# Optimization experiments

Measured on AMD Instinct MI355X. Metric: run time of the kernel, lower is better.

## Reference

```python
import jax, jax.numpy as jnp
import numpy as np

# NSAFlowLayer config (from init_kwargs)
W_ORTHO = 0.5      # w: blend weight of soft-polar retraction
MAX_ITER = 50      # max_iter (run fixed-length under jit; tol check omitted)
LR = 0.1           # 'default' initial learning rate for the fidelity gradient step
NS_ITERS = 8       # Newton-Schulz iterations for the (k,k) inverse matrix sqrt
EPS = 1e-8

B, P, K = 32, 16384, 64


def _invsqrt_ns(M):
    """Differentiable inverse sqrt of SPD (k,k) matrix via coupled Newton-Schulz."""
    k = M.shape[0]
    I = jnp.eye(k, dtype=M.dtype)
    nrm = jnp.trace(M) + EPS
    Y = M / nrm
    Z = I
    for _ in range(NS_ITERS):  # small fixed loop over k x k mats
        T = 0.5 * (3.0 * I - Z @ Y)
        Y = Y @ T
        Z = T @ Z
    return Z / jnp.sqrt(nrm)  # approx M^{-1/2}


def _nsa_flow_single(x0):
    """One independent NSA flow: gradient step on 0.5||Y-X0||^2, soft-polar
    retraction toward the Stiefel manifold, nonnegativity projection."""
    def step(Y, _):
        G = Y - x0                      # fidelity gradient (p,k)
        Y = Y - LR * G                  # gradient step
        S = _invsqrt_ns(Y.T @ Y)        # (k,k) inverse sqrt of Gram matrix
        Y = (1.0 - W_ORTHO) * Y + W_ORTHO * (Y @ S)  # soft polar retraction
        Y = jnp.maximum(Y, 0.0)         # nonneg projection
        return Y, None
    Yf, _ = jax.lax.scan(step, x0, None, length=MAX_ITER)  # Y0 = X0
    return Yf


def setup_inputs() -> dict:
    key = jax.random.key(0)
    X0 = jax.random.uniform(key, (B, P, K), dtype=jnp.float32)
    return {"X0": X0}


def reference(X0) -> jnp.ndarray:
    return jax.vmap(_nsa_flow_single)(X0)  # (B, p, k)
```

## Files before the change

### kernel.cpp

```cpp
#include <hip/hip_runtime.h>


#define BATCH 32
#define NP    16384
#define NK    64
#define NITER 50
#define NSIT  8
#define EPSC  1e-8f

#define BPB   16
#define RPB   (NP / BPB)
#define CH    64
#define NCH   (RPB / CH)
#define NBLK  (BATCH * BPB)
#define NT    256

#define FMA16(D, A0, A1, A2, A3, BV) do {                                  \
  D[0][0] = fmaf(A0, BV.x, D[0][0]); D[0][1] = fmaf(A0, BV.y, D[0][1]);    \
  D[0][2] = fmaf(A0, BV.z, D[0][2]); D[0][3] = fmaf(A0, BV.w, D[0][3]);    \
  D[1][0] = fmaf(A1, BV.x, D[1][0]); D[1][1] = fmaf(A1, BV.y, D[1][1]);    \
  D[1][2] = fmaf(A1, BV.z, D[1][2]); D[1][3] = fmaf(A1, BV.w, D[1][3]);    \
  D[2][0] = fmaf(A2, BV.x, D[2][0]); D[2][1] = fmaf(A2, BV.y, D[2][1]);    \
  D[2][2] = fmaf(A2, BV.z, D[2][2]); D[2][3] = fmaf(A2, BV.w, D[2][3]);    \
  D[3][0] = fmaf(A3, BV.x, D[3][0]); D[3][1] = fmaf(A3, BV.y, D[3][1]);    \
  D[3][2] = fmaf(A3, BV.z, D[3][2]); D[3][3] = fmaf(A3, BV.w, D[3][3]);    \
} while (0)

__device__ __forceinline__ void gram_acc(const float (*sZ)[NK], int i0, int j0,
                                         float (&acc)[4][4]) {
#pragma unroll 4
  for (int r = 0; r < CH; ++r) {
    float4 zi = *(const float4*)&sZ[r][i0];
    float4 zj = *(const float4*)&sZ[r][j0];
    FMA16(acc, zi.x, zi.y, zi.z, zi.w, zj);
  }
}

__global__ __launch_bounds__(NT, 2) void k_init(const float* __restrict__ X0,
                                                float* __restrict__ Y,
                                                float* __restrict__ partials) {
  __shared__ float sZ[CH][NK];
  const int tid = threadIdx.x, blk = blockIdx.x;
  const int b = blk >> 4, rb = blk & 15;
  const size_t base = ((size_t)b * NP + (size_t)rb * RPB) * NK;
  const float* __restrict__ x0 = X0 + base;
  float* __restrict__ y = Y + base;
  const int it = tid >> 4, jt = tid & 15;
  const int i0 = it * 4, j0 = jt * 4;
  float acc[4][4] = {{0.f}};

  for (int ch = 0; ch < NCH; ++ch) {
    const float* xo = x0 + ch * CH * NK;
    float* yo = y + ch * CH * NK;
#pragma unroll
    for (int q = 0; q < 4; ++q) {
      int fi = (q * NT + tid) * 4;
      float4 xv = *(const float4*)(xo + fi);
      *(float4*)(yo + fi) = xv;
      int r = fi >> 6, c = fi & 63;
      *(float4*)&sZ[r][c] = xv;
    }
    __syncthreads();
    gram_acc(sZ, i0, j0, acc);
    __syncthreads();
  }
  float* p = partials + (size_t)blk * NK * NK;
#pragma unroll
  for (int a = 0; a < 4; ++a)
    *(float4*)(p + (i0 + a) * NK + j0) =
        make_float4(acc[a][0], acc[a][1], acc[a][2], acc[a][3]);
}

__global__ void k_ns(const float* __restrict__ partials, float* __restrict__ S) {
  __shared__ float sA[NK][68];
  __shared__ float sB[NK][68];
  __shared__ float sT[NK][68];
  __shared__ float sRed[16];

  const int tid = threadIdx.x, b = blockIdx.x;
  const int it = tid >> 4, jt = tid & 15;
  const int i0 = it * 4, j0 = jt * 4;

  float m[4][4] = {{0.f}};
  const float* pb = partials + (size_t)b * BPB * NK * NK;
#pragma unroll
  for (int p = 0; p < BPB; ++p) {
    const float* pp = pb + p * NK * NK;
#pragma unroll
    for (int a = 0; a < 4; ++a) {
      float4 v = *(const float4*)(pp + (i0 + a) * NK + j0);
      m[a][0] += v.x; m[a][1] += v.y; m[a][2] += v.z; m[a][3] += v.w;
    }
  }
  if (it == jt) sRed[it] = m[0][0] + m[1][1] + m[2][2] + m[3][3];
  __syncthreads();
  float nrm = EPSC;
#pragma unroll
  for (int i = 0; i < 16; ++i) nrm += sRed[i];
  const float inv = 1.0f / nrm;

#pragma unroll
  for (int a = 0; a < 4; ++a)
#pragma unroll
    for (int c = 0; c < 4; ++c) {
      sA[i0 + a][j0 + c] = m[a][c] * inv;
      sB[i0 + a][j0 + c] = (i0 + a) == (j0 + c) ? 1.0f : 0.0f;
    }
  __syncthreads();

  for (int ns = 0; ns < NSIT; ++ns) {
    float d[4][4] = {{0.f}};
#pragma unroll 4
    for (int k = 0; k < NK; ++k) {
      float b0 = sB[i0 + 0][k], b1 = sB[i0 + 1][k];
      float b2 = sB[i0 + 2][k], b3 = sB[i0 + 3][k];
      float4 av = *(const float4*)&sA[k][j0];
      FMA16(d, b0, b1, b2, b3, av);
    }
#pragma unroll
    for (int a = 0; a < 4; ++a)
#pragma unroll
      for (int c = 0; c < 4; ++c)
        sT[i0 + a][j0 + c] =
            (((i0 + a) == (j0 + c)) ? 1.5f : 0.0f) - 0.5f * d[a][c];
    __syncthreads();

    float r1[4][4] = {{0.f}}, r2[4][4] = {{0.f}};
#pragma unroll 4
    for (int k = 0; k < NK; ++k) {
      float y0 = sA[i0 + 0][k], y1 = sA[i0 + 1][k];
      float y2 = sA[i0 + 2][k], y3 = sA[i0 + 3][k];
      float4 tv = *(const float4*)&sT[k][j0];
      FMA16(r1, y0, y1, y2, y3, tv);
      float t0 = sT[i0 + 0][k], t1 = sT[i0 + 1][k];
      float t2 = sT[i0 + 2][k], t3 = sT[i0 + 3][k];
      float4 zv = *(const float4*)&sB[k][j0];
      FMA16(r2, t0, t1, t2, t3, zv);
    }
    __syncthreads();
#pragma unroll
    for (int a = 0; a < 4; ++a)
#pragma unroll
      for (int c = 0; c < 4; ++c) {
        sA[i0 + a][j0 + c] = r1[a][c];
        sB[i0 + a][j0 + c] = r2[a][c];
      }
    __syncthreads();
  }

  const float sc = 1.0f / sqrtf(nrm);
  float* Sb = S + (size_t)b * NK * NK;
#pragma unroll
  for (int a = 0; a < 4; ++a) {
    float4 v = make_float4(sB[i0 + a][j0 + 0] * sc, sB[i0 + a][j0 + 1] * sc,
                           sB[i0 + a][j0 + 2] * sc, sB[i0 + a][j0 + 3] * sc);
    *(float4*)(Sb + (i0 + a) * NK + j0) = v;
  }
}

__global__ __launch_bounds__(NT, 2) void k_fused(const float* __restrict__ X0,
                                                 float* __restrict__ Y,
                                                 const float* __restrict__ S,
                                                 float* __restrict__ partials,
                                                 int last) {
  __shared__ float sS[NK][NK];
  __shared__ float sYp[CH][NK + 1];
  __shared__ float sZ[CH][NK];

  const int tid = threadIdx.x, blk = blockIdx.x;
  const int b = blk >> 4, rb = blk & 15;
  const size_t base = ((size_t)b * NP + (size_t)rb * RPB) * NK;
  const float* __restrict__ x0 = X0 + base;
  float* __restrict__ y = Y + base;

  {
    const float4* Sb = (const float4*)(S + (size_t)b * NK * NK);
    float4* d = (float4*)sS;
    for (int i = tid; i < NK * NK / 4; i += NT) d[i] = Sb[i];
  }

  const int it = tid >> 4, jt = tid & 15;
  const int i0 = it * 4, j0 = jt * 4;
  float acc[4][4] = {{0.f}};
  __syncthreads();

  for (int ch = 0; ch < NCH; ++ch) {
    const float* xo = x0 + ch * CH * NK;
    float* yo = y + ch * CH * NK;

#pragma unroll
    for (int q = 0; q < 4; ++q) {
      int fi = (q * NT + tid) * 4;
      int r = fi >> 6, c = fi & 63;
      float4 yv = *(const float4*)(yo + fi);
      float4 xv = *(const float4*)(xo + fi);
      sYp[r][c + 0] = fmaf(0.9f, yv.x, 0.1f * xv.x);
      sYp[r][c + 1] = fmaf(0.9f, yv.y, 0.1f * xv.y);
      sYp[r][c + 2] = fmaf(0.9f, yv.z, 0.1f * xv.z);
      sYp[r][c + 3] = fmaf(0.9f, yv.w, 0.1f * xv.w);
    }
    __syncthreads();

    float dot[4][4] = {{0.f}};
#pragma unroll 4
    for (int k = 0; k < NK; ++k) {
      float a0 = sYp[i0 + 0][k], a1 = sYp[i0 + 1][k];
      float a2 = sYp[i0 + 2][k], a3 = sYp[i0 + 3][k];
      float4 bv = *(const float4*)&sS[k][j0];
      FMA16(dot, a0, a1, a2, a3, bv);
    }

#pragma unroll
    for (int a = 0; a < 4; ++a) {
      int r = i0 + a;
      float4 yn;
      yn.x = fmaxf(fmaf(0.5f, sYp[r][j0 + 0], 0.5f * dot[a][0]), 0.f);
      yn.y = fmaxf(fmaf(0.5f, sYp[r][j0 + 1], 0.5f * dot[a][1]), 0.f);
      yn.z = fmaxf(fmaf(0.5f, sYp[r][j0 + 2], 0.5f * dot[a][2]), 0.f);
      yn.w = fmaxf(fmaf(0.5f, sYp[r][j0 + 3], 0.5f * dot[a][3]), 0.f);
      *(float4*)(yo + r * NK + j0) = yn;
      if (!last) {
        float4 xv = *(const float4*)(xo + r * NK + j0);
        float4 z;
        z.x = fmaf(0.9f, yn.x, 0.1f * xv.x);
        z.y = fmaf(0.9f, yn.y, 0.1f * xv.y);
        z.z = fmaf(0.9f, yn.z, 0.1f * xv.z);
        z.w = fmaf(0.9f, yn.w, 0.1f * xv.w);
        *(float4*)&sZ[r][j0] = z;
      }
    }
    __syncthreads();
    if (!last) gram_acc(sZ, i0, j0, acc);
    __syncthreads();
  }

  if (!last) {
    float* p = partials + (size_t)blk * NK * NK;
#pragma unroll
    for (int a = 0; a < 4; ++a)
      *(float4*)(p + (i0 + a) * NK + j0) =
          make_float4(acc[a][0], acc[a][1], acc[a][2], acc[a][3]);
  }
}

extern "C" void kernel_launch(void* const* d_in, const int* in_sizes, int n_in,
                              void* d_out, int out_size, void* d_ws,
                              size_t ws_size, hipStream_t stream) {
  (void)in_sizes; (void)n_in; (void)out_size; (void)ws_size;
  const float* X0 = (const float*)d_in[0];
  float* Y = (float*)d_out;
  float* partials = (float*)d_ws;
  float* S = partials + (size_t)NBLK * NK * NK;

  k_init<<<NBLK, NT, 0, stream>>>(X0, Y, partials);
  for (int t = 0; t < NITER; ++t) {
    k_ns<<<BATCH, NT, 0, stream>>>(partials, S);
    k_fused<<<NBLK, NT, 0, stream>>>(X0, Y, S, partials, t == NITER - 1 ? 1 : 0);
  }
}
```

Before: 10.58 ms.

## Double row-blocks per batch, widen NS kernel, reuse LDS buffer, peel first NS step

When the workspace is large enough, each batch's P rows are split across 32 blocks instead of 16, doubling the grid so more CUs stay busy. LDS use in the fused kernel drops by reusing the sYp buffer for the Gram input, and occupancy bounds rise to 4 blocks per CU. The Newton-Schulz kernel now runs 512 threads with 2x4 tiles, reduces the trace with a wave shuffle, and peels the first iteration since Z starts as the identity. In exchange there are twice as many partial Gram matrices to sum, plus an extra barrier per chunk, and the fast path depends on the workspace size.

```diff
diff --git a/kernel.cpp b/kernel.cpp
--- a/kernel.cpp
+++ b/kernel.cpp
@@ -7,13 +7,10 @@
 #define NITER 50
 #define NSIT  8
 #define EPSC  1e-8f
-
-#define BPB   16
-#define RPB   (NP / BPB)
 #define CH    64
-#define NCH   (RPB / CH)
-#define NBLK  (BATCH * BPB)
 #define NT    256
+#define NTNS  512
+#define SP    68
 
 #define FMA16(D, A0, A1, A2, A3, BV) do {                                  \
   D[0][0] = fmaf(A0, BV.x, D[0][0]); D[0][1] = fmaf(A0, BV.y, D[0][1]);    \
@@ -26,7 +23,14 @@
   D[3][2] = fmaf(A3, BV.z, D[3][2]); D[3][3] = fmaf(A3, BV.w, D[3][3]);    \
 } while (0)
 
-__device__ __forceinline__ void gram_acc(const float (*sZ)[NK], int i0, int j0,
+#define FMA8(D, A0, A1, BV) do {                                           \
+  D[0][0] = fmaf(A0, BV.x, D[0][0]); D[0][1] = fmaf(A0, BV.y, D[0][1]);    \
+  D[0][2] = fmaf(A0, BV.z, D[0][2]); D[0][3] = fmaf(A0, BV.w, D[0][3]);    \
+  D[1][0] = fmaf(A1, BV.x, D[1][0]); D[1][1] = fmaf(A1, BV.y, D[1][1]);    \
+  D[1][2] = fmaf(A1, BV.z, D[1][2]); D[1][3] = fmaf(A1, BV.w, D[1][3]);    \
+} while (0)
+
+__device__ __forceinline__ void gram_acc(const float (*sZ)[SP], int i0, int j0,
                                          float (&acc)[4][4]) {
 #pragma unroll 4
   for (int r = 0; r < CH; ++r) {
@@ -36,20 +40,23 @@
   }
 }
 
-__global__ __launch_bounds__(NT, 2) void k_init(const float* __restrict__ X0,
+__global__ __launch_bounds__(NT, 4) void k_init(const float* __restrict__ X0,
                                                 float* __restrict__ Y,
-                                                float* __restrict__ partials) {
-  __shared__ float sZ[CH][NK];
+                                                float* __restrict__ partials,
+                                                int shift) {
+  __shared__ float sZ[CH][SP];
   const int tid = threadIdx.x, blk = blockIdx.x;
-  const int b = blk >> 4, rb = blk & 15;
-  const size_t base = ((size_t)b * NP + (size_t)rb * RPB) * NK;
+  const int bpb = 1 << shift;
+  const int b = blk >> shift, rb = blk & (bpb - 1);
+  const int rpb = NP >> shift, nch = rpb / CH;
+  const size_t base = ((size_t)b * NP + (size_t)rb * rpb) * NK;
   const float* __restrict__ x0 = X0 + base;
   float* __restrict__ y = Y + base;
   const int it = tid >> 4, jt = tid & 15;
   const int i0 = it * 4, j0 = jt * 4;
   float acc[4][4] = {{0.f}};
 
-  for (int ch = 0; ch < NCH; ++ch) {
+  for (int ch = 0; ch < nch; ++ch) {
     const float* xo = x0 + ch * CH * NK;
     float* yo = y + ch * CH * NK;
 #pragma unroll
@@ -71,36 +78,46 @@
         make_float4(acc[a][0], acc[a][1], acc[a][2], acc[a][3]);
 }
 
-__global__ void k_ns(const float* __restrict__ partials, float* __restrict__ S) {
-  __shared__ float sA[NK][68];
-  __shared__ float sB[NK][68];
-  __shared__ float sT[NK][68];
-  __shared__ float sRed[16];
+__global__ __launch_bounds__(NTNS, 2) void k_ns(const float* __restrict__ partials,
+                                                float* __restrict__ S,
+                                                int npart) {
+  __shared__ float sA[NK][SP];
+  __shared__ float sB[NK][SP];
+  __shared__ float sT[NK][SP];
+  __shared__ float sRed[8];
 
   const int tid = threadIdx.x, b = blockIdx.x;
   const int it = tid >> 4, jt = tid & 15;
-  const int i0 = it * 4, j0 = jt * 4;
-
-  float m[4][4] = {{0.f}};
-  const float* pb = partials + (size_t)b * BPB * NK * NK;
-#pragma unroll
-  for (int p = 0; p < BPB; ++p) {
+  const int i0 = it * 2, j0 = jt * 4;
+
+  float m[2][4] = {{0.f}};
+  const float* pb = partials + (size_t)b * npart * NK * NK;
+#pragma unroll 4
+  for (int p = 0; p < npart; ++p) {
     const float* pp = pb + p * NK * NK;
 #pragma unroll
-    for (int a = 0; a < 4; ++a) {
+    for (int a = 0; a < 2; ++a) {
       float4 v = *(const float4*)(pp + (i0 + a) * NK + j0);
       m[a][0] += v.x; m[a][1] += v.y; m[a][2] += v.z; m[a][3] += v.w;
     }
   }
-  if (it == jt) sRed[it] = m[0][0] + m[1][1] + m[2][2] + m[3][3];
+  float local = 0.f;
+#pragma unroll
+  for (int a = 0; a < 2; ++a)
+#pragma unroll
+    for (int c = 0; c < 4; ++c)
+      if ((i0 + a) == (j0 + c)) local += m[a][c];
+#pragma unroll
+  for (int off = 32; off; off >>= 1) local += __shfl_down(local, off);
+  if ((tid & 63) == 0) sRed[tid >> 6] = local;
   __syncthreads();
   float nrm = EPSC;
 #pragma unroll
-  for (int i = 0; i < 16; ++i) nrm += sRed[i];
+  for (int w = 0; w < 8; ++w) nrm += sRed[w];
   const float inv = 1.0f / nrm;
 
 #pragma unroll
-  for (int a = 0; a < 4; ++a)
+  for (int a = 0; a < 2; ++a)
 #pragma unroll
     for (int c = 0; c < 4; ++c) {
       sA[i0 + a][j0 + c] = m[a][c] * inv;
@@ -108,38 +125,61 @@
     }
   __syncthreads();
 
-  for (int ns = 0; ns < NSIT; ++ns) {
-    float d[4][4] = {{0.f}};
+  {
+#pragma unroll
+    for (int a = 0; a < 2; ++a)
+#pragma unroll
+      for (int c = 0; c < 4; ++c)
+        sT[i0 + a][j0 + c] =
+            (((i0 + a) == (j0 + c)) ? 1.5f : 0.0f) - 0.5f * sA[i0 + a][j0 + c];
+    __syncthreads();
+    float r1[2][4] = {{0.f}};
+#pragma unroll 4
+    for (int k = 0; k < NK; ++k) {
+      float y0 = sA[i0 + 0][k], y1 = sA[i0 + 1][k];
+      float4 tv = *(const float4*)&sT[k][j0];
+      FMA8(r1, y0, y1, tv);
+    }
+    __syncthreads();
+#pragma unroll
+    for (int a = 0; a < 2; ++a)
+#pragma unroll
+      for (int c = 0; c < 4; ++c) {
+        sA[i0 + a][j0 + c] = r1[a][c];
+        sB[i0 + a][j0 + c] = sT[i0 + a][j0 + c];
+      }
+    __syncthreads();
+  }
+
+  for (int ns = 1; ns < NSIT; ++ns) {
+    float d[2][4] = {{0.f}};
 #pragma unroll 4
     for (int k = 0; k < NK; ++k) {
       float b0 = sB[i0 + 0][k], b1 = sB[i0 + 1][k];
-      float b2 = sB[i0 + 2][k], b3 = sB[i0 + 3][k];
       float4 av = *(const float4*)&sA[k][j0];
-      FMA16(d, b0, b1, b2, b3, av);
-    }
-#pragma unroll
-    for (int a = 0; a < 4; ++a)
+      FMA8(d, b0, b1, av);
+    }
+#pragma unroll
+    for (int a = 0; a < 2; ++a)
 #pragma unroll
       for (int c = 0; c < 4; ++c)
         sT[i0 + a][j0 + c] =
             (((i0 + a) == (j0 + c)) ? 1.5f : 0.0f) - 0.5f * d[a][c];
     __syncthreads();
 
-    float r1[4][4] = {{0.f}}, r2[4][4] = {{0.f}};
+    float r1[2][4] = {{0.f}}, r2[2][4] = {{0.f}};
 #pragma unroll 4
     for (int k = 0; k < NK; ++k) {
       float y0 = sA[i0 + 0][k], y1 = sA[i0 + 1][k];
-      float y2 = sA[i0 + 2][k], y3 = sA[i0 + 3][k];
       float4 tv = *(const float4*)&sT[k][j0];
-      FMA16(r1, y0, y1, y2, y3, tv);
+      FMA8(r1, y0, y1, tv);
       float t0 = sT[i0 + 0][k], t1 = sT[i0 + 1][k];
-      float t2 = sT[i0 + 2][k], t3 = sT[i0 + 3][k];
       float4 zv = *(const float4*)&sB[k][j0];
-      FMA16(r2, t0, t1, t2, t3, zv);
-    }
-    __syncthreads();
-#pragma unroll
-    for (int a = 0; a < 4; ++a)
+      FMA8(r2, t0, t1, zv);
+    }
+    __syncthreads();
+#pragma unroll
+    for (int a = 0; a < 2; ++a)
 #pragma unroll
       for (int c = 0; c < 4; ++c) {
         sA[i0 + a][j0 + c] = r1[a][c];
@@ -151,25 +191,26 @@
   const float sc = 1.0f / sqrtf(nrm);
   float* Sb = S + (size_t)b * NK * NK;
 #pragma unroll
-  for (int a = 0; a < 4; ++a) {
+  for (int a = 0; a < 2; ++a) {
     float4 v = make_float4(sB[i0 + a][j0 + 0] * sc, sB[i0 + a][j0 + 1] * sc,
                            sB[i0 + a][j0 + 2] * sc, sB[i0 + a][j0 + 3] * sc);
     *(float4*)(Sb + (i0 + a) * NK + j0) = v;
   }
 }
 
-__global__ __launch_bounds__(NT, 2) void k_fused(const float* __restrict__ X0,
+__global__ __launch_bounds__(NT, 4) void k_fused(const float* __restrict__ X0,
                                                  float* __restrict__ Y,
                                                  const float* __restrict__ S,
                                                  float* __restrict__ partials,
-                                                 int last) {
+                                                 int last, int shift) {
   __shared__ float sS[NK][NK];
-  __shared__ float sYp[CH][NK + 1];
-  __shared__ float sZ[CH][NK];
+  __shared__ float sYp[CH][SP];
 
   const int tid = threadIdx.x, blk = blockIdx.x;
-  const int b = blk >> 4, rb = blk & 15;
-  const size_t base = ((size_t)b * NP + (size_t)rb * RPB) * NK;
+  const int bpb = 1 << shift;
+  const int b = blk >> shift, rb = blk & (bpb - 1);
+  const int rpb = NP >> shift, nch = rpb / CH;
+  const size_t base = ((size_t)b * NP + (size_t)rb * rpb) * NK;
   const float* __restrict__ x0 = X0 + base;
   float* __restrict__ y = Y + base;
 
@@ -184,7 +225,7 @@
   float acc[4][4] = {{0.f}};
   __syncthreads();
 
-  for (int ch = 0; ch < NCH; ++ch) {
+  for (int ch = 0; ch < nch; ++ch) {
     const float* xo = x0 + ch * CH * NK;
     float* yo = y + ch * CH * NK;
 
@@ -194,10 +235,12 @@
       int r = fi >> 6, c = fi & 63;
       float4 yv = *(const float4*)(yo + fi);
       float4 xv = *(const float4*)(xo + fi);
-      sYp[r][c + 0] = fmaf(0.9f, yv.x, 0.1f * xv.x);
-      sYp[r][c + 1] = fmaf(0.9f, yv.y, 0.1f * xv.y);
-      sYp[r][c + 2] = fmaf(0.9f, yv.z, 0.1f * xv.z);
-      sYp[r][c + 3] = fmaf(0.9f, yv.w, 0.1f * xv.w);
+      float4 yp;
+      yp.x = fmaf(0.9f, yv.x, 0.1f * xv.x);
+      yp.y = fmaf(0.9f, yv.y, 0.1f * xv.y);
+      yp.z = fmaf(0.9f, yv.z, 0.1f * xv.z);
+      yp.w = fmaf(0.9f, yv.w, 0.1f * xv.w);
+      *(float4*)&sYp[r][c] = yp;
     }
     __syncthreads();
 
@@ -209,15 +252,17 @@
       float4 bv = *(const float4*)&sS[k][j0];
       FMA16(dot, a0, a1, a2, a3, bv);
     }
+    __syncthreads();
 
 #pragma unroll
     for (int a = 0; a < 4; ++a) {
       int r = i0 + a;
+      float4 ypv = *(const float4*)&sYp[r][j0];
       float4 yn;
-      yn.x = fmaxf(fmaf(0.5f, sYp[r][j0 + 0], 0.5f * dot[a][0]), 0.f);
-      yn.y = fmaxf(fmaf(0.5f, sYp[r][j0 + 1], 0.5f * dot[a][1]), 0.f);
-      yn.z = fmaxf(fmaf(0.5f, sYp[r][j0 + 2], 0.5f * dot[a][2]), 0.f);
-      yn.w = fmaxf(fmaf(0.5f, sYp[r][j0 + 3], 0.5f * dot[a][3]), 0.f);
+      yn.x = fmaxf(fmaf(0.5f, ypv.x, 0.5f * dot[a][0]), 0.f);
+      yn.y = fmaxf(fmaf(0.5f, ypv.y, 0.5f * dot[a][1]), 0.f);
+      yn.z = fmaxf(fmaf(0.5f, ypv.z, 0.5f * dot[a][2]), 0.f);
+      yn.w = fmaxf(fmaf(0.5f, ypv.w, 0.5f * dot[a][3]), 0.f);
       *(float4*)(yo + r * NK + j0) = yn;
       if (!last) {
         float4 xv = *(const float4*)(xo + r * NK + j0);
@@ -226,11 +271,11 @@
         z.y = fmaf(0.9f, yn.y, 0.1f * xv.y);
         z.z = fmaf(0.9f, yn.z, 0.1f * xv.z);
         z.w = fmaf(0.9f, yn.w, 0.1f * xv.w);
-        *(float4*)&sZ[r][j0] = z;
+        *(float4*)&sYp[r][j0] = z;
       }
     }
     __syncthreads();
-    if (!last) gram_acc(sZ, i0, j0, acc);
+    if (!last) gram_acc(sYp, i0, j0, acc);
     __syncthreads();
   }
 
@@ -246,15 +291,22 @@
 extern "C" void kernel_launch(void* const* d_in, const int* in_sizes, int n_in,
                               void* d_out, int out_size, void* d_ws,
                               size_t ws_size, hipStream_t stream) {
-  (void)in_sizes; (void)n_in; (void)out_size; (void)ws_size;
+  (void)in_sizes; (void)n_in; (void)out_size;
   const float* X0 = (const float*)d_in[0];
   float* Y = (float*)d_out;
+
+  const size_t needed5 =
+      ((size_t)(BATCH << 5) + BATCH) * NK * NK * sizeof(float);
+  const int shift = (ws_size >= needed5) ? 5 : 4;
+  const int nblk = BATCH << shift;
+
   float* partials = (float*)d_ws;
-  float* S = partials + (size_t)NBLK * NK * NK;
-
-  k_init<<<NBLK, NT, 0, stream>>>(X0, Y, partials);
+  float* S = partials + (size_t)nblk * NK * NK;
+
+  k_init<<<nblk, NT, 0, stream>>>(X0, Y, partials, shift);
   for (int t = 0; t < NITER; ++t) {
-    k_ns<<<BATCH, NT, 0, stream>>>(partials, S);
-    k_fused<<<NBLK, NT, 0, stream>>>(X0, Y, S, partials, t == NITER - 1 ? 1 : 0);
-  }
-}
+    k_ns<<<BATCH, NTNS, 0, stream>>>(partials, S, 1 << shift);
+    k_fused<<<nblk, NT, 0, stream>>>(X0, Y, S, partials,
+                                     t == NITER - 1 ? 1 : 0, shift);
+  }
+}
```

New measurement: 9.877 ms. 1.07x faster.
